# Kernel tuning notes

Hardware: AMD Instinct MI355X
Metric: run time of the kernel (lower is better)

Reference implementation:

```python
import jax, jax.numpy as jnp
import numpy as np

N, K = 2000, 16          # nodes, neighbors per node (uniform-degree KNN graph)
C_S, C_Z, NUM_RBF = 128, 64, 64
EPS = 1e-8
D_MIN, D_MAX = 0.0, 20.0  # standard protein RBF range


def setup_inputs() -> dict:
    key = jax.random.key(0)
    ks = jax.random.split(key, 16)
    E = N * K
    node_features = jax.random.normal(ks[0], (N, C_S), dtype=jnp.float32)
    trans = jax.random.normal(ks[1], (N, 3), dtype=jnp.float32) * 10.0
    edge_features = jax.random.normal(ks[2], (E, C_Z), dtype=jnp.float32)
    # sorted-by-destination, uniform degree: dest = repeat(arange(N), K); src random
    src = jax.random.randint(ks[3], (E,), 0, N)
    dst = jnp.repeat(jnp.arange(E // K), K)
    edge_index = jnp.stack([src, dst]).astype(jnp.int64)
    s = 0.05
    return {
        "node_features": node_features,
        "trans": trans,
        "edge_features": edge_features,
        "edge_index": edge_index,
        "w_gate": jax.random.normal(ks[4], (2 * C_S, C_Z), dtype=jnp.float32) * s,
        "b_gate": jnp.zeros((C_Z,), jnp.float32),
        "w_db": jax.random.normal(ks[5], (NUM_RBF, C_Z), dtype=jnp.float32) * s,
        "b_db": jnp.zeros((C_Z,), jnp.float32),
        "w_edge": jax.random.normal(ks[6], (C_Z, C_Z), dtype=jnp.float32) * s,
        "b_edge": jnp.zeros((C_Z,), jnp.float32),
        "ln_g": jnp.ones((C_Z,), jnp.float32),
        "ln_b": jnp.zeros((C_Z,), jnp.float32),
        "w_out": jax.random.normal(ks[7], (C_Z, C_Z), dtype=jnp.float32) * s,
        "b_out": jnp.zeros((C_Z,), jnp.float32),
    }


def _rbf(d):
    # d: [...]; returns [..., NUM_RBF]
    mu = jnp.linspace(D_MIN, D_MAX, NUM_RBF, dtype=d.dtype)
    sigma = (D_MAX - D_MIN) / NUM_RBF
    return jnp.exp(-(((d[..., None] - mu) / sigma) ** 2))


def _layernorm(x, g, b, eps=1e-5):
    m = jnp.mean(x, axis=-1, keepdims=True)
    v = jnp.var(x, axis=-1, keepdims=True)
    return (x - m) * jax.lax.rsqrt(v + eps) * g + b


def reference(node_features, trans, edge_features, edge_index,
              w_gate, b_gate, w_db, b_db, w_edge, b_edge,
              ln_g, ln_b, w_out, b_out):
    n = node_features.shape[0]
    k = edge_index.shape[1] // n
    # sparse -> dense KNN blocks (uniform degree, sorted by destination)
    knn_idx = edge_index[0].reshape(n, k)                 # [n,k] source nodes
    knn_feats = edge_features.reshape(n, k, -1)           # [n,k,c_z]

    # gather node features for all (i,j) neighbor pairs
    nf = node_features[knn_idx]                           # [n,k,c_s]
    nf_i = jnp.broadcast_to(nf[:, :, None, :], (n, k, k, nf.shape[-1]))
    nf_j = jnp.broadcast_to(nf[:, None, :, :], (n, k, k, nf.shape[-1]))
    pair = jnp.concatenate([nf_i, nf_j], axis=-1)         # [n,k,k,2*c_s]
    gate = jax.nn.sigmoid(pair @ w_gate + b_gate)         # [n,k,k,c_z]

    # pairwise distances between neighbor translations
    t = trans[knn_idx]                                    # [n,k,3]
    diff = t[:, :, None, :] - t[:, None, :, :] + EPS
    dist = jnp.linalg.norm(diff, axis=-1)                 # [n,k,k]
    dist_bias = gate * (_rbf(dist) @ w_db + b_db)         # [n,k,k,c_z]

    kf = knn_feats @ w_edge + b_edge                      # [n,k,c_z]
    upd = jnp.einsum('nijh,nih->njh', dist_bias, kf)      # [n,k,c_z]
    upd = _layernorm(upd, ln_g, ln_b)

    # dense KNN -> sparse edge list, final projection
    upd = upd.reshape(n * k, -1)                          # [E,c_z]
    return upd @ w_out + b_out
```

## Files before the change

kernel.cpp:

```cpp
#include <hip/hip_runtime.h>
#include <hip/hip_bf16.h>

#define NND 2000
#define KNB 16
#define CS 128
#define CZ 64
#define NE (NND*KNB)

typedef __attribute__((ext_vector_type(8))) short short8;
typedef __attribute__((ext_vector_type(4))) float f32x4;
typedef __attribute__((ext_vector_type(2))) unsigned int uint2v;
typedef __attribute__((ext_vector_type(4))) unsigned int uint4v;

__device__ __forceinline__ unsigned int pk2(float a, float b) {
  __hip_bfloat162 h = __float22bfloat162_rn(make_float2(a, b));
  unsigned int u;
  __builtin_memcpy(&u, &h, 4);
  return u;
}
__device__ __forceinline__ unsigned short bfc(float f) {
  __hip_bfloat16 h = __float2bfloat16(f);
  unsigned short u;
  __builtin_memcpy(&u, &h, 2);
  return u;
}

__device__ __forceinline__ float fexp2(float x) {
#if __has_builtin(__builtin_amdgcn_exp2f)
  return __builtin_amdgcn_exp2f(x);
#else
  return __expf(0.6931471805599453f * x);
#endif
}

__global__ __launch_bounds__(256) void precompute_kernel(
    const float* __restrict__ nf,
    const float* __restrict__ w_gate, const float* __restrict__ b_gate,
    const float* __restrict__ ln_b, const float* __restrict__ w_out,
    const float* __restrict__ b_out,
    const float* __restrict__ w_db, const float* __restrict__ w_edge,
    const float* __restrict__ ln_g,
    float* __restrict__ g1, float* __restrict__ g2, float* __restrict__ bias2,
    unsigned short* __restrict__ wdbF, unsigned short* __restrict__ wedF,
    unsigned short* __restrict__ woF)
{
  __shared__ float wl[2*CS][CZ];
  const int p = threadIdx.x;
  const int lane = p & 63;
  const int wv   = p >> 6;
  const int b    = blockIdx.x;
  if (b < NND/4) {
    #pragma unroll
    for (int t = 0; t < 16; ++t) {
      const int e = (p + 256*t) * 4;
      const f32x4 x = *(const f32x4*)&w_gate[e];
      *(f32x4*)&wl[e >> 6][e & 63] = x;
    }
    __syncthreads();

    const int v = b*4 + wv;
    const float* nrow = nf + v*CS;
    float a10=0.f,a11=0.f,a12=0.f,a13=0.f;
    float a20=0.f,a21=0.f,a22=0.f,a23=0.f;
    #pragma unroll
    for (int cc = 0; cc < CS; cc += 4) {
      const f32x4 x = *(const f32x4*)&nrow[cc];
      a10 = fmaf(x[0], wl[cc+0][lane], a10);
      a11 = fmaf(x[1], wl[cc+1][lane], a11);
      a12 = fmaf(x[2], wl[cc+2][lane], a12);
      a13 = fmaf(x[3], wl[cc+3][lane], a13);
      a20 = fmaf(x[0], wl[CS+cc+0][lane], a20);
      a21 = fmaf(x[1], wl[CS+cc+1][lane], a21);
      a22 = fmaf(x[2], wl[CS+cc+2][lane], a22);
      a23 = fmaf(x[3], wl[CS+cc+3][lane], a23);
    }
    const float a1 = b_gate[lane] + ((a10+a11)+(a12+a13));
    const float a2 = (a20+a21)+(a22+a23);
    g1[v*CZ + lane] = fexp2(a1 * -1.4426950408889634f);
    g2[v*CZ + lane] = fexp2(a2 * -1.4426950408889634f);
  } else {
    if (wv == 0) {
      float a = b_out[lane];
      #pragma unroll
      for (int cc = 0; cc < CZ; ++cc)
        a = fmaf(ln_b[cc], w_out[cc*CZ + lane], a);
      bias2[lane] = a;
    } else if (wv == 1) {
      for (int e = lane; e < 4096; e += 64) {
        const int entry = e >> 3, t = e & 7;
        const int l2 = entry & 63, sn = entry >> 6;
        const int s = sn >> 2, nt = sn & 3;
        const int q2 = l2 >> 4, c2 = l2 & 15;
        wdbF[e] = bfc(w_db[(32*s + 8*q2 + t)*CZ + 16*nt + c2]);
      }
    } else if (wv == 2) {
      for (int e = lane; e < 4096; e += 64) {
        const int entry = e >> 3, t = e & 7;
        const int p2 = entry & 255, s = entry >> 8;
        const int q2 = (p2 >> 4) & 3, c2 = p2 & 15;
        wedF[e] = bfc(w_edge[(32*s + 8*q2 + t)*CZ + 16*(p2 >> 6) + c2]);
      }
    } else {
      for (int e = lane; e < 4096; e += 64) {
        const int entry = e >> 3, t = e & 7;
        const int p2 = entry & 255, s = entry >> 8;
        const int q2 = (p2 >> 4) & 3, c2 = p2 & 15;
        const int k = 32*s + 8*q2 + t;
        woF[e] = bfc(w_out[k*CZ + 16*(p2 >> 6) + c2] * ln_g[k]);
      }
    }
  }
}

__global__ __launch_bounds__(256, 4) void fused_main_kernel(
    const float* __restrict__ trans, const int* __restrict__ eidx,
    const float* __restrict__ g1, const float* __restrict__ g2,
    const float* __restrict__ ef, const float* __restrict__ b_edge,
    const float* __restrict__ b_db, const float* __restrict__ bias2,
    const unsigned short* __restrict__ wdbF,
    const unsigned short* __restrict__ wedF,
    const unsigned short* __restrict__ woF,
    float* __restrict__ out)
{
  __shared__ float G1l[KNB][68];
  __shared__ float G2l[KNB][68];
  __shared__ float kfl[KNB][68];
  __shared__ unsigned short xh[KNB][72];

  const int n = blockIdx.x;
  const int p = threadIdx.x;
  const int w = p >> 6;
  const int l = p & 63;
  const int q = l >> 4;
  const int c = l & 15;
  const int r16 = p >> 4, c4 = (p & 15) * 4;

  const int sr = eidx[n*KNB + r16];
  const int sc = eidx[n*KNB + c];
  int sj[4];
  #pragma unroll
  for (int m = 0; m < 4; ++m) sj[m] = eidx[n*KNB + 4*w + m];

  const f32x4 g1row = *(const f32x4*)&g1[sr*CZ + c4];
  const f32x4 g2row = *(const f32x4*)&g2[sr*CZ + c4];
  const f32x4 efrow = *(const f32x4*)&ef[(n*KNB + r16)*CZ + c4];

  const float tc0 = trans[sc*3+0], tc1 = trans[sc*3+1], tc2 = trans[sc*3+2];
  float tj[4][3];
  #pragma unroll
  for (int m = 0; m < 4; ++m) {
    tj[m][0] = trans[sj[m]*3+0];
    tj[m][1] = trans[sj[m]*3+1];
    tj[m][2] = trans[sj[m]*3+2];
  }

  short8 wed[2];
  #pragma unroll
  for (int s = 0; s < 2; ++s)
    wed[s] = *(const short8*)&wedF[(s*256 + p)*8];
  short8 bcur[2];
  #pragma unroll
  for (int s = 0; s < 2; ++s)
    bcur[s] = *(const short8*)&wdbF[(s*4*64 + l)*8];

  const float be = b_edge[16*w + c];
  const float bo = bias2[16*w + c];
  float bdb[4];
  #pragma unroll
  for (int nt = 0; nt < 4; ++nt) bdb[nt] = b_db[16*nt + c];

  const float STEP = 1.2201878439258035f;
  float dsc[4];
  #pragma unroll
  for (int m = 0; m < 4; ++m) {
    const float dx = tc0 - tj[m][0] + 1e-8f;
    const float dy = tc1 - tj[m][1] + 1e-8f;
    const float dz = tc2 - tj[m][2] + 1e-8f;
    dsc[m] = sqrtf(fmaf(dx,dx, fmaf(dy,dy, dz*dz))) * 3.8435917081166394f;
  }
  const float qoff = (float)(8*q) * STEP;

  short8 af[2][4];
  #pragma unroll
  for (int s = 0; s < 2; ++s) {
    const float soff = qoff + (float)(32*s) * STEP;
    #pragma unroll
    for (int m = 0; m < 4; ++m) {
      const float bse = dsc[m] - soff;
      uint4v u;
      #pragma unroll
      for (int t = 0; t < 4; ++t) {
        const float ua = fmaf(-STEP, (float)(2*t),   bse);
        const float ub = fmaf(-STEP, (float)(2*t+1), bse);
        u[t] = pk2(fexp2(-ua*ua), fexp2(-ub*ub));
      }
      short8 v;
      __builtin_memcpy(&v, &u, 16);
      af[s][m] = v;
    }
  }

  {
    uint2v pk;
    pk[0] = pk2(efrow[0], efrow[1]);
    pk[1] = pk2(efrow[2], efrow[3]);
    *(uint2v*)&xh[r16][c4] = pk;
    *(f32x4*)&G1l[r16][c4] = g1row;
    *(f32x4*)&G2l[r16][c4] = g2row;
  }
  __syncthreads();

  {
    f32x4 ak = {};
    #pragma unroll
    for (int s = 0; s < 2; ++s) {
      const short8 a0 = *(const short8*)&xh[c][q*8 + 32*s];
      ak = __builtin_amdgcn_mfma_f32_16x16x32_bf16(a0, wed[s], ak, 0, 0, 0);
    }
    #pragma unroll
    for (int r = 0; r < 4; ++r)
      kfl[4*q + r][16*w + c] = ak[r] + be;
  }
  __syncthreads();

  float upd[4][4];
  #pragma unroll
  for (int nt = 0; nt < 4; ++nt) {
    short8 bnext[2];
    if (nt < 3) {
      #pragma unroll
      for (int s = 0; s < 2; ++s)
        bnext[s] = *(const short8*)&wdbF[((s*4 + nt+1)*64 + l)*8];
    }
    float e1v[4], kfv[4];
    #pragma unroll
    for (int r = 0; r < 4; ++r) {
      e1v[r] = G1l[4*q + r][16*nt + c];
      kfv[r] = kfl[4*q + r][16*nt + c];
    }
    const float bdbn = bdb[nt];
    f32x4 acc[4];
    #pragma unroll
    for (int m = 0; m < 4; ++m) acc[m] = (f32x4){bdbn, bdbn, bdbn, bdbn};
    #pragma unroll
    for (int s = 0; s < 2; ++s)
      #pragma unroll
      for (int m = 0; m < 4; ++m)
        acc[m] = __builtin_amdgcn_mfma_f32_16x16x32_bf16(af[s][m], bcur[s], acc[m], 0, 0, 0);

    #pragma unroll
    for (int m = 0; m < 4; ++m) {
      const float e2m = G2l[4*w + m][16*nt + c];
      float ss = 0.f;
      #pragma unroll
      for (int r = 0; r < 4; ++r) {
        const float gate = __builtin_amdgcn_rcpf(fmaf(e1v[r], e2m, 1.0f));
        ss = fmaf(gate * acc[m][r], kfv[r], ss);
      }
      ss += __shfl_xor(ss, 16);
      ss += __shfl_xor(ss, 32);
      upd[m][nt] = ss;
    }
    if (nt < 3) { bcur[0] = bnext[0]; bcur[1] = bnext[1]; }
  }

  short8 wb[2];
  #pragma unroll
  for (int s = 0; s < 2; ++s)
    wb[s] = *(const short8*)&woF[(s*256 + p)*8];

  {
    float v[4];
    #pragma unroll
    for (int nt = 0; nt < 4; ++nt)
      v[nt] = (q == 0) ? upd[0][nt] : (q == 1) ? upd[1][nt]
            : (q == 2) ? upd[2][nt] : upd[3][nt];
    float s1 = (v[0] + v[1]) + (v[2] + v[3]);
    float s2 = fmaf(v[0],v[0], fmaf(v[1],v[1], fmaf(v[2],v[2], v[3]*v[3])));
    #pragma unroll
    for (int mk = 1; mk <= 8; mk <<= 1) {
      s1 += __shfl_xor(s1, mk);
      s2 += __shfl_xor(s2, mk);
    }
    const float mean = s1 * 0.015625f;
    const float var  = fmaf(s2, 0.015625f, -mean*mean);
    const float rstd = rsqrtf(var + 1e-5f);
    #pragma unroll
    for (int nt = 0; nt < 4; ++nt)
      xh[4*w + q][16*nt + c] = bfc((v[nt] - mean) * rstd);
  }
  __syncthreads();

  f32x4 acc2 = {};
  #pragma unroll
  for (int s = 0; s < 2; ++s) {
    const short8 a2f = *(const short8*)&xh[c][q*8 + 32*s];
    acc2 = __builtin_amdgcn_mfma_f32_16x16x32_bf16(a2f, wb[s], acc2, 0, 0, 0);
  }
  #pragma unroll
  for (int r = 0; r < 4; ++r)
    out[(n*KNB + 4*q + r)*CZ + 16*w + c] = acc2[r] + bo;
}

extern "C" void kernel_launch(void* const* d_in, const int* in_sizes, int n_in,
                              void* d_out, int out_size, void* d_ws, size_t ws_size,
                              hipStream_t stream)
{
  const float* nf     = (const float*)d_in[0];
  const float* trans  = (const float*)d_in[1];
  const float* ef     = (const float*)d_in[2];
  const int*   eidx   = (const int*)d_in[3];
  const float* w_gate = (const float*)d_in[4];
  const float* b_gate = (const float*)d_in[5];
  const float* w_db   = (const float*)d_in[6];
  const float* b_db   = (const float*)d_in[7];
  const float* w_edge = (const float*)d_in[8];
  const float* b_edge = (const float*)d_in[9];
  const float* ln_g   = (const float*)d_in[10];
  const float* ln_b   = (const float*)d_in[11];
  const float* w_out  = (const float*)d_in[12];
  const float* b_out  = (const float*)d_in[13];
  float* out = (float*)d_out;

  float* g1    = (float*)d_ws;
  float* g2    = g1 + NND*CZ;
  float* bias2 = g2 + NND*CZ;
  unsigned short* wdbF = (unsigned short*)(bias2 + CZ);
  unsigned short* wedF = wdbF + 4096;
  unsigned short* woF  = wedF + 4096;

  precompute_kernel<<<NND/4 + 1, 256, 0, stream>>>(
      nf, w_gate, b_gate, ln_b, w_out, b_out, w_db, w_edge, ln_g,
      g1, g2, bias2, wdbF, wedF, woF);
  fused_main_kernel<<<NND, 256, 0, stream>>>(
      trans, eidx, g1, g2, ef, b_edge, b_db, bias2,
      wdbF, wedF, woF, out);
}
```

Baseline: 30.96 us.

## Load gate/edge operands directly into registers and drop shared-memory staging barriers

Each wave now gathers its own g1/g2 rows straight from global memory into registers and computes the full edge-feature projection kf redundantly per wave with four MFMAs, removing the G1l/G2l/kfl shared arrays and two __syncthreads. This removes LDS round-trips and block-wide barriers before the main RBF loop. In exchange it adds redundant global loads and MFMA work per wave and more register pressure, so launch bounds are relaxed from 4 to 3 blocks per CU.

```diff
diff --git a/kernel.cpp b/kernel.cpp
--- a/kernel.cpp
+++ b/kernel.cpp
@@ -112,7 +112,7 @@
   }
 }
 
-__global__ __launch_bounds__(256, 4) void fused_main_kernel(
+__global__ __launch_bounds__(256, 3) void fused_main_kernel(
     const float* __restrict__ trans, const int* __restrict__ eidx,
     const float* __restrict__ g1, const float* __restrict__ g2,
     const float* __restrict__ ef, const float* __restrict__ b_edge,
@@ -122,9 +122,6 @@
     const unsigned short* __restrict__ woF,
     float* __restrict__ out)
 {
-  __shared__ float G1l[KNB][68];
-  __shared__ float G2l[KNB][68];
-  __shared__ float kfl[KNB][68];
   __shared__ unsigned short xh[KNB][72];
 
   const int n = blockIdx.x;
@@ -133,41 +130,72 @@
   const int l = p & 63;
   const int q = l >> 4;
   const int c = l & 15;
-  const int r16 = p >> 4, c4 = (p & 15) * 4;
-
-  const int sr = eidx[n*KNB + r16];
-  const int sc = eidx[n*KNB + c];
-  int sj[4];
-  #pragma unroll
-  for (int m = 0; m < 4; ++m) sj[m] = eidx[n*KNB + 4*w + m];
-
-  const f32x4 g1row = *(const f32x4*)&g1[sr*CZ + c4];
-  const f32x4 g2row = *(const f32x4*)&g2[sr*CZ + c4];
-  const f32x4 efrow = *(const f32x4*)&ef[(n*KNB + r16)*CZ + c4];
+  const int base = n*KNB;
+
+  const int4 eq = *(const int4*)&eidx[base + 4*q];
+  const int4 ej = *(const int4*)&eidx[base + 4*w];
+  const int  sc = eidx[base + c];
+
+  const int eqa[4] = {eq.x, eq.y, eq.z, eq.w};
+  const int eja[4] = {ej.x, ej.y, ej.z, ej.w};
+
+  float e1v[4][4], e2v[4][4];
+  #pragma unroll
+  for (int nt = 0; nt < 4; ++nt)
+    #pragma unroll
+    for (int r = 0; r < 4; ++r) {
+      e1v[nt][r] = g1[eqa[r]*CZ + 16*nt + c];
+      e2v[nt][r] = g2[eja[r]*CZ + 16*nt + c];
+    }
 
   const float tc0 = trans[sc*3+0], tc1 = trans[sc*3+1], tc2 = trans[sc*3+2];
   float tj[4][3];
   #pragma unroll
   for (int m = 0; m < 4; ++m) {
-    tj[m][0] = trans[sj[m]*3+0];
-    tj[m][1] = trans[sj[m]*3+1];
-    tj[m][2] = trans[sj[m]*3+2];
-  }
-
-  short8 wed[2];
-  #pragma unroll
-  for (int s = 0; s < 2; ++s)
-    wed[s] = *(const short8*)&wedF[(s*256 + p)*8];
+    tj[m][0] = trans[eja[m]*3+0];
+    tj[m][1] = trans[eja[m]*3+1];
+    tj[m][2] = trans[eja[m]*3+2];
+  }
+
+  short8 afe[2];
+  #pragma unroll
+  for (int s = 0; s < 2; ++s) {
+    const float* src = &ef[(base + c)*CZ + 32*s + 8*q];
+    const f32x4 x0 = *(const f32x4*)src;
+    const f32x4 x1 = *(const f32x4*)(src + 4);
+    uint4v u;
+    u[0] = pk2(x0[0], x0[1]);
+    u[1] = pk2(x0[2], x0[3]);
+    u[2] = pk2(x1[0], x1[1]);
+    u[3] = pk2(x1[2], x1[3]);
+    short8 v;
+    __builtin_memcpy(&v, &u, 16);
+    afe[s] = v;
+  }
+
   short8 bcur[2];
   #pragma unroll
   for (int s = 0; s < 2; ++s)
     bcur[s] = *(const short8*)&wdbF[(s*4*64 + l)*8];
 
-  const float be = b_edge[16*w + c];
   const float bo = bias2[16*w + c];
   float bdb[4];
   #pragma unroll
   for (int nt = 0; nt < 4; ++nt) bdb[nt] = b_db[16*nt + c];
+
+  f32x4 kfc[4];
+  #pragma unroll
+  for (int cb = 0; cb < 4; ++cb) {
+    const float be = b_edge[16*cb + c];
+    kfc[cb] = (f32x4){be, be, be, be};
+  }
+  #pragma unroll
+  for (int s = 0; s < 2; ++s)
+    #pragma unroll
+    for (int cb = 0; cb < 4; ++cb) {
+      const short8 wed = *(const short8*)&wedF[(s*256 + cb*64 + l)*8];
+      kfc[cb] = __builtin_amdgcn_mfma_f32_16x16x32_bf16(afe[s], wed, kfc[cb], 0, 0, 0);
+    }
 
   const float STEP = 1.2201878439258035f;
   float dsc[4];
@@ -179,7 +207,6 @@
     dsc[m] = sqrtf(fmaf(dx,dx, fmaf(dy,dy, dz*dz))) * 3.8435917081166394f;
   }
   const float qoff = (float)(8*q) * STEP;
-
   short8 af[2][4];
   #pragma unroll
   for (int s = 0; s < 2; ++s) {
@@ -200,29 +227,6 @@
     }
   }
 
-  {
-    uint2v pk;
-    pk[0] = pk2(efrow[0], efrow[1]);
-    pk[1] = pk2(efrow[2], efrow[3]);
-    *(uint2v*)&xh[r16][c4] = pk;
-    *(f32x4*)&G1l[r16][c4] = g1row;
-    *(f32x4*)&G2l[r16][c4] = g2row;
-  }
-  __syncthreads();
-
-  {
-    f32x4 ak = {};
-    #pragma unroll
-    for (int s = 0; s < 2; ++s) {
-      const short8 a0 = *(const short8*)&xh[c][q*8 + 32*s];
-      ak = __builtin_amdgcn_mfma_f32_16x16x32_bf16(a0, wed[s], ak, 0, 0, 0);
-    }
-    #pragma unroll
-    for (int r = 0; r < 4; ++r)
-      kfl[4*q + r][16*w + c] = ak[r] + be;
-  }
-  __syncthreads();
-
   float upd[4][4];
   #pragma unroll
   for (int nt = 0; nt < 4; ++nt) {
@@ -232,12 +236,6 @@
       for (int s = 0; s < 2; ++s)
         bnext[s] = *(const short8*)&wdbF[((s*4 + nt+1)*64 + l)*8];
     }
-    float e1v[4], kfv[4];
-    #pragma unroll
-    for (int r = 0; r < 4; ++r) {
-      e1v[r] = G1l[4*q + r][16*nt + c];
-      kfv[r] = kfl[4*q + r][16*nt + c];
-    }
     const float bdbn = bdb[nt];
     f32x4 acc[4];
     #pragma unroll
@@ -250,12 +248,12 @@
 
     #pragma unroll
     for (int m = 0; m < 4; ++m) {
-      const float e2m = G2l[4*w + m][16*nt + c];
+      const float e2m = e2v[nt][m];
       float ss = 0.f;
       #pragma unroll
       for (int r = 0; r < 4; ++r) {
-        const float gate = __builtin_amdgcn_rcpf(fmaf(e1v[r], e2m, 1.0f));
-        ss = fmaf(gate * acc[m][r], kfv[r], ss);
+        const float gate = __builtin_amdgcn_rcpf(fmaf(e1v[nt][r], e2m, 1.0f));
+        ss = fmaf(gate * acc[m][r], kfc[nt][r], ss);
       }
       ss += __shfl_xor(ss, 16);
       ss += __shfl_xor(ss, 32);
@@ -299,7 +297,7 @@
   }
   #pragma unroll
   for (int r = 0; r < 4; ++r)
-    out[(n*KNB + 4*q + r)*CZ + 16*w + c] = acc2[r] + bo;
+    out[(base + 4*q + r)*CZ + 16*w + c] = acc2[r] + bo;
 }
 
 extern "C" void kernel_launch(void* const* d_in, const int* in_sizes, int n_in,
```

Result: slower. 34.27 us (+10.7%).
